# Kernel tuning notes

Hardware: AMD Instinct MI355X
Metric: run time of the kernel (lower is better)

Reference implementation:

```python
import jax, jax.numpy as jnp
import numpy as np

# CaMoE_Block MoE dispatch/combine reference.
# Assumptions (undefined submodules in source): RWKV7_TimeMix/att residual omitted
# (h = ln2(x) directly); SparseRWKVFFN experts modeled as RWKV channel-mix FFNs
# y = relu(h @ W1)^2 @ W2; the LinearTransformerExpert (last expert) uses the same
# FFN form with recon_loss = 0; per-expert confidence head conf_e = sigmoid(h @ wc_e + bc_e).
# Faithful parts: winner selection, winning-bid lookup, straight-through scale
# factor conf / (stop_grad(conf) + 1e-6), per-expert compute, scatter-combine, residual.

B, T, C = 4, 2048, 1024
E = 5            # num_rwkv_experts + 1
H = 4 * C        # FFN hidden
LN_EPS = 1e-5


def setup_inputs() -> dict:
    key = jax.random.key(0)
    ks = jax.random.split(key, 8)
    x = jax.random.normal(ks[0], (B, T, C), dtype=jnp.float32)
    winners = jax.random.randint(ks[1], (B, T), 0, E)
    gamma = jnp.ones((C,), jnp.float32)
    beta = jnp.zeros((C,), jnp.float32)
    w1 = jax.random.normal(ks[2], (E, C, H), jnp.float32) * (1.0 / np.sqrt(C))
    w2 = jax.random.normal(ks[3], (E, H, C), jnp.float32) * (1.0 / np.sqrt(H))
    wc = jax.random.normal(ks[4], (E, C), jnp.float32) * (1.0 / np.sqrt(C))
    bc = jnp.zeros((E,), jnp.float32)
    return {"x": x, "winners": winners, "gamma": gamma, "beta": beta,
            "w1": w1, "w2": w2, "wc": wc, "bc": bc}


def _layernorm(x, gamma, beta):
    mu = jnp.mean(x, axis=-1, keepdims=True)
    var = jnp.mean(jnp.square(x - mu), axis=-1, keepdims=True)
    return (x - mu) * jax.lax.rsqrt(var + LN_EPS) * gamma + beta


def reference(x, winners, gamma, beta, w1, w2, wc, bc):
    b, t, c = x.shape
    e = w1.shape[0]
    h = _layernorm(x, gamma, beta)
    hf = h.reshape(-1, c)                     # [N, C]
    win = winners.reshape(-1)                 # [N]

    # per-expert confidences (bids)
    conf = jax.nn.sigmoid(hf @ wc.T + bc)     # [N, E]
    winning_bids = jnp.take_along_axis(conf, win[:, None], axis=1)  # [N, 1]
    scale = winning_bids / (jax.lax.stop_gradient(winning_bids) + 1e-6)

    # dense all-expert FFN (squared-ReLU channel mix), then top-1 select
    k = jnp.square(jax.nn.relu(jnp.einsum('nc,ech->enh', hf, w1)))  # [E, N, H]
    y = jnp.einsum('enh,ehc->enc', k, w2)                            # [E, N, C]
    sel = jax.nn.one_hot(win, e, dtype=y.dtype)                      # [N, E]
    expert_out = jnp.einsum('ne,enc->nc', sel, y)                    # scatter-combine

    out = (expert_out * scale).reshape(b, t, c)
    return x + out
```

## Files before the change

### kernel.cpp

```cpp
#include <hip/hip_runtime.h>
#include <hip/hip_bf16.h>
#include <stdint.h>

#define N_TOK 8192
#define C_DIM 1024
#define H_DIM 4096
#define E_NUM 5
#define LN_EPS 1e-5f

typedef __hip_bfloat16 bf16;
using s8v = __attribute__((ext_vector_type(8))) short;
using f4v = __attribute__((ext_vector_type(4))) float;

__device__ __forceinline__ void async_ld16(const bf16* g, bf16* l) {
    __builtin_amdgcn_global_load_lds(
        (const __attribute__((address_space(1))) void*)g,
        (__attribute__((address_space(3))) void*)l,
        16, 0, 0);
}

__global__ void init_meta_kernel(int* meta) {
    if (threadIdx.x < 16) meta[threadIdx.x] = 0;
}

__global__ __launch_bounds__(256) void count_kernel(
    const int* __restrict__ win, int* __restrict__ meta)
{
    __shared__ int c[E_NUM];
    if (threadIdx.x < E_NUM) c[threadIdx.x] = 0;
    __syncthreads();
    int n = blockIdx.x * 256 + threadIdx.x;
    atomicAdd(&c[win[n]], 1);
    __syncthreads();
    if (threadIdx.x < E_NUM) atomicAdd(&meta[threadIdx.x], c[threadIdx.x]);
}

__global__ void scan_kernel(int* meta) {
    if (threadIdx.x == 0) {
        int off = 0;
        for (int e = 0; e < E_NUM; ++e) {
            meta[5 + e] = off;
            off += meta[e];
            meta[11 + e] = 0;
        }
        meta[5 + E_NUM] = off;
    }
}

__global__ __launch_bounds__(256) void scatter_kernel(
    const int* __restrict__ win, int* __restrict__ meta,
    int* __restrict__ idx, int* __restrict__ pos)
{
    __shared__ int c[E_NUM];
    __shared__ int base[E_NUM];
    if (threadIdx.x < E_NUM) c[threadIdx.x] = 0;
    __syncthreads();
    int n = blockIdx.x * 256 + threadIdx.x;
    int e = win[n];
    int lr = atomicAdd(&c[e], 1);
    __syncthreads();
    if (threadIdx.x < E_NUM)
        base[threadIdx.x] = atomicAdd(&meta[11 + threadIdx.x], c[threadIdx.x]);
    __syncthreads();
    int p = meta[5 + e] + base[e] + lr;
    idx[p] = n;
    pos[n] = p;
}

__global__ __launch_bounds__(256) void ln_conf_kernel(
    const float* __restrict__ x, const int* __restrict__ win,
    const float* __restrict__ gamma, const float* __restrict__ beta,
    const float* __restrict__ wc, const float* __restrict__ bc,
    const int* __restrict__ pos,
    bf16* __restrict__ hbuf, float* __restrict__ scl,
    float* __restrict__ out)
{
    int n = blockIdx.x;
    int t = threadIdx.x;
    const float* xr = x + (size_t)n * C_DIM;
    float v[4];
    float s = 0.f, ss = 0.f;
#pragma unroll
    for (int i = 0; i < 4; ++i) {
        v[i] = xr[t + i * 256];
        s += v[i];
        ss += v[i] * v[i];
    }
#pragma unroll
    for (int off = 32; off > 0; off >>= 1) {
        s  += __shfl_down(s, off);
        ss += __shfl_down(ss, off);
    }
    __shared__ float red[8];
    __shared__ float mu_s, rv_s;
    int wave = t >> 6, lane = t & 63;
    if (lane == 0) { red[wave] = s; red[4 + wave] = ss; }
    __syncthreads();
    if (t == 0) {
        float S  = red[0] + red[1] + red[2] + red[3];
        float SS = red[4] + red[5] + red[6] + red[7];
        float mu = S * (1.f / C_DIM);
        float var = SS * (1.f / C_DIM) - mu * mu;
        mu_s = mu;
        rv_s = rsqrtf(var + LN_EPS);
    }
    __syncthreads();
    float mu = mu_s, rv = rv_s;
    int e = win[n];
    int p = pos[n];
    const float* wce = wc + (size_t)e * C_DIM;
    float dot = 0.f;
#pragma unroll
    for (int i = 0; i < 4; ++i) {
        int ci = t + i * 256;
        float hv = (v[i] - mu) * rv * gamma[ci] + beta[ci];
        hbuf[(size_t)p * C_DIM + ci] = (bf16)hv;
        out[(size_t)n * C_DIM + ci] = v[i];
        dot += hv * wce[ci];
    }
#pragma unroll
    for (int off = 32; off > 0; off >>= 1) dot += __shfl_down(dot, off);
    if (lane == 0) red[wave] = dot;
    __syncthreads();
    if (t == 0) {
        float z = red[0] + red[1] + red[2] + red[3] + bc[e];
        float conf = 1.f / (1.f + expf(-z));
        scl[p] = conf / (conf + 1e-6f);
    }
}

__global__ __launch_bounds__(256) void transpose_cvt_kernel(
    const float* __restrict__ src, bf16* __restrict__ dst, int R, int S)
{
    __shared__ float tile[64][65];
    size_t ebase = (size_t)blockIdx.z * (size_t)R * (size_t)S;
    int s0 = blockIdx.x * 64;
    int r0 = blockIdx.y * 64;
    int t = threadIdx.x;
    int lr = t >> 4;
    int lc = (t & 15) * 4;
#pragma unroll
    for (int i = 0; i < 4; ++i) {
        int r = lr + i * 16;
        float4 v = *(const float4*)(src + ebase + (size_t)(r0 + r) * S + s0 + lc);
        tile[r][lc + 0] = v.x;
        tile[r][lc + 1] = v.y;
        tile[r][lc + 2] = v.z;
        tile[r][lc + 3] = v.w;
    }
    __syncthreads();
    int sc = t >> 2;
#pragma unroll
    for (int p = 0; p < 2; ++p) {
        int ch = (t & 3) + p * 4;
        bf16 vals[8];
#pragma unroll
        for (int j = 0; j < 8; ++j)
            vals[j] = (bf16)tile[ch * 8 + j][sc];
        *(s8v*)(dst + ebase + (size_t)(s0 + sc) * R + r0 + ch * 8) = *(s8v*)vals;
    }
}


__global__ __launch_bounds__(256) void gemm1_kernel(
    const bf16* __restrict__ hbuf, const bf16* __restrict__ w1t,
    const int* __restrict__ meta, bf16* __restrict__ ks)
{
    int e = blockIdx.z;
    int base_p = meta[5 + e];
    int cnt = meta[6 + e] - base_p;
    int m0 = blockIdx.y * 128;
    if (m0 >= cnt) return;
    int n0 = blockIdx.x * 128;

    __shared__ __align__(16) bf16 As[128 * 32];
    __shared__ __align__(16) bf16 Bs[128 * 32];

    int t = threadIdx.x;
    int lane = t & 63;
    int wv = t >> 6;
    int wr = wv >> 1, wcol = wv & 1;

    int i0 = (t & 7) ^ ((t >> 3) & 7);
    int srow = 2 * (t >> 3) + (i0 >> 2);
    int schk = i0 & 3;

    int r1 = min(m0 + srow, cnt - 1);
    int r2 = min(m0 + 64 + srow, cnt - 1);
    const bf16* ga1 = hbuf + (size_t)(base_p + r1) * C_DIM + schk * 8;
    const bf16* ga2 = hbuf + (size_t)(base_p + r2) * C_DIM + schk * 8;
    const bf16* wbase = w1t + (size_t)e * H_DIM * C_DIM;
    const bf16* gb1 = wbase + (size_t)(n0 + srow) * C_DIM + schk * 8;
    const bf16* gb2 = wbase + (size_t)(n0 + 64 + srow) * C_DIM + schk * 8;

    bf16* la1 = As + t * 8;
    bf16* la2 = As + 2048 + t * 8;
    bf16* lb1 = Bs + t * 8;
    bf16* lb2 = Bs + 2048 + t * 8;

    int kq = lane >> 4;
    int rhalf = (lane & 15) >> 1;
    int ifrag = ((lane & 1) << 2) | kq;
    int foff = rhalf * 64 + (ifrag ^ rhalf) * 8;
    const bf16* Af = As + wr * 2048 + foff;
    const bf16* Bf = Bs + wcol * 2048 + foff;

    f4v acc[4][4];
    f4v zero = {0.f, 0.f, 0.f, 0.f};
#pragma unroll
    for (int i = 0; i < 4; ++i)
#pragma unroll
        for (int j = 0; j < 4; ++j) acc[i][j] = zero;

    for (int kb = 0; kb < C_DIM / 32; ++kb) {
        __syncthreads();
        async_ld16(ga1, la1); ga1 += 32;
        async_ld16(ga2, la2); ga2 += 32;
        async_ld16(gb1, lb1); gb1 += 32;
        async_ld16(gb2, lb2); gb2 += 32;
        __syncthreads();
        s8v af[4], bfv[4];
#pragma unroll
        for (int mi = 0; mi < 4; ++mi)
            af[mi] = *(const s8v*)(Af + mi * 512);
#pragma unroll
        for (int ni = 0; ni < 4; ++ni)
            bfv[ni] = *(const s8v*)(Bf + ni * 512);
#pragma unroll
        for (int mi = 0; mi < 4; ++mi)
#pragma unroll
            for (int ni = 0; ni < 4; ++ni)
                acc[mi][ni] = __builtin_amdgcn_mfma_f32_16x16x32_bf16(af[mi], bfv[ni], acc[mi][ni], 0, 0, 0);
    }

#pragma unroll
    for (int mi = 0; mi < 4; ++mi) {
#pragma unroll
        for (int r = 0; r < 4; ++r) {
            int row_local = wr * 64 + mi * 16 + ((lane >> 4) << 2) + r;
            int gm = m0 + row_local;
            if (gm < cnt) {
                size_t p = (size_t)(base_p + gm);
#pragma unroll
                for (int ni = 0; ni < 4; ++ni) {
                    int col = n0 + wcol * 64 + ni * 16 + (lane & 15);
                    float v = acc[mi][ni][r];
                    float rl = fmaxf(v, 0.f);
                    ks[p * H_DIM + col] = (bf16)(rl * rl);
                }
            }
        }
    }
}

__global__ __launch_bounds__(256) void gemm2_kernel(
    const bf16* __restrict__ ks, const bf16* __restrict__ w2t,
    const int* __restrict__ idx, const int* __restrict__ meta,
    const float* __restrict__ scl, float* __restrict__ out)
{
    int z = blockIdx.z;
    int e = z >> 1;
    int kh = z & 1;
    int base_p = meta[5 + e];
    int cnt = meta[6 + e] - base_p;
    int m0 = blockIdx.y * 128;
    if (m0 >= cnt) return;
    int n0 = blockIdx.x * 128;
    int kbase = kh * (H_DIM / 2);

    __shared__ __align__(16) bf16 As[128 * 32];
    __shared__ __align__(16) bf16 Bs[128 * 32];

    int t = threadIdx.x;
    int lane = t & 63;
    int wv = t >> 6;
    int wr = wv >> 1, wcol = wv & 1;

    int i0 = (t & 7) ^ ((t >> 3) & 7);
    int srow = 2 * (t >> 3) + (i0 >> 2);
    int schk = i0 & 3;

    int r1 = min(m0 + srow, cnt - 1);
    int r2 = min(m0 + 64 + srow, cnt - 1);
    const bf16* ga1 = ks + (size_t)(base_p + r1) * H_DIM + kbase + schk * 8;
    const bf16* ga2 = ks + (size_t)(base_p + r2) * H_DIM + kbase + schk * 8;
    const bf16* wbase = w2t + (size_t)e * C_DIM * H_DIM;
    const bf16* gb1 = wbase + (size_t)(n0 + srow) * H_DIM + kbase + schk * 8;
    const bf16* gb2 = wbase + (size_t)(n0 + 64 + srow) * H_DIM + kbase + schk * 8;

    bf16* la1 = As + t * 8;
    bf16* la2 = As + 2048 + t * 8;
    bf16* lb1 = Bs + t * 8;
    bf16* lb2 = Bs + 2048 + t * 8;

    int kq = lane >> 4;
    int rhalf = (lane & 15) >> 1;
    int ifrag = ((lane & 1) << 2) | kq;
    int foff = rhalf * 64 + (ifrag ^ rhalf) * 8;
    const bf16* Af = As + wr * 2048 + foff;
    const bf16* Bf = Bs + wcol * 2048 + foff;

    f4v acc[4][4];
    f4v zero = {0.f, 0.f, 0.f, 0.f};
#pragma unroll
    for (int i = 0; i < 4; ++i)
#pragma unroll
        for (int j = 0; j < 4; ++j) acc[i][j] = zero;

    for (int kb = 0; kb < (H_DIM / 2) / 32; ++kb) {
        __syncthreads();
        async_ld16(ga1, la1); ga1 += 32;
        async_ld16(ga2, la2); ga2 += 32;
        async_ld16(gb1, lb1); gb1 += 32;
        async_ld16(gb2, lb2); gb2 += 32;
        __syncthreads();
        s8v af[4], bfv[4];
#pragma unroll
        for (int mi = 0; mi < 4; ++mi)
            af[mi] = *(const s8v*)(Af + mi * 512);
#pragma unroll
        for (int ni = 0; ni < 4; ++ni)
            bfv[ni] = *(const s8v*)(Bf + ni * 512);
#pragma unroll
        for (int mi = 0; mi < 4; ++mi)
#pragma unroll
            for (int ni = 0; ni < 4; ++ni)
                acc[mi][ni] = __builtin_amdgcn_mfma_f32_16x16x32_bf16(af[mi], bfv[ni], acc[mi][ni], 0, 0, 0);
    }

#pragma unroll
    for (int mi = 0; mi < 4; ++mi) {
        int tok[4];
        float sclv[4];
#pragma unroll
        for (int r = 0; r < 4; ++r) {
            int row_local = wr * 64 + mi * 16 + ((lane >> 4) << 2) + r;
            int gm = m0 + row_local;
            if (gm < cnt) {
                tok[r] = idx[base_p + gm];
                sclv[r] = scl[base_p + gm];
            } else {
                tok[r] = -1;
                sclv[r] = 0.f;
            }
        }
#pragma unroll
        for (int ni = 0; ni < 4; ++ni) {
            int col = n0 + wcol * 64 + ni * 16 + (lane & 15);
#pragma unroll
            for (int r = 0; r < 4; ++r) {
                if (tok[r] >= 0) {
                    size_t o = (size_t)tok[r] * C_DIM + col;
                    atomicAdd(&out[o], acc[mi][ni][r] * sclv[r]);
                }
            }
        }
    }
}

extern "C" void kernel_launch(void* const* d_in, const int* in_sizes, int n_in,
                              void* d_out, int out_size, void* d_ws, size_t ws_size,
                              hipStream_t stream) {
    const float* x     = (const float*)d_in[0];
    const int*   win   = (const int*)d_in[1];
    const float* gamma = (const float*)d_in[2];
    const float* beta  = (const float*)d_in[3];
    const float* w1    = (const float*)d_in[4];
    const float* w2    = (const float*)d_in[5];
    const float* wc    = (const float*)d_in[6];
    const float* bc    = (const float*)d_in[7];
    float* out = (float*)d_out;

    char* ws = (char*)d_ws;
    size_t o = 0;
    bf16* w1t  = (bf16*)(ws + o); o += (size_t)E_NUM * H_DIM * C_DIM * 2;
    bf16* w2t  = (bf16*)(ws + o); o += (size_t)E_NUM * C_DIM * H_DIM * 2;
    bf16* hbuf = (bf16*)(ws + o); o += (size_t)N_TOK * C_DIM * 2;
    bf16* ks   = (bf16*)(ws + o); o += (size_t)N_TOK * H_DIM * 2;
    float* scl = (float*)(ws + o); o += (size_t)N_TOK * 4;
    int* idx   = (int*)(ws + o);   o += (size_t)N_TOK * 4;
    int* pos   = (int*)(ws + o);   o += (size_t)N_TOK * 4;
    int* meta  = (int*)(ws + o);   o += 64;

    hipLaunchKernelGGL(init_meta_kernel, dim3(1), dim3(64), 0, stream, meta);
    hipLaunchKernelGGL(count_kernel, dim3(N_TOK / 256), dim3(256), 0, stream, win, meta);
    hipLaunchKernelGGL(scan_kernel, dim3(1), dim3(64), 0, stream, meta);
    hipLaunchKernelGGL(scatter_kernel, dim3(N_TOK / 256), dim3(256), 0, stream, win, meta, idx, pos);
    hipLaunchKernelGGL(transpose_cvt_kernel, dim3(H_DIM / 64, C_DIM / 64, E_NUM), dim3(256), 0, stream,
                       w1, w1t, C_DIM, H_DIM);
    hipLaunchKernelGGL(transpose_cvt_kernel, dim3(C_DIM / 64, H_DIM / 64, E_NUM), dim3(256), 0, stream,
                       w2, w2t, H_DIM, C_DIM);
    hipLaunchKernelGGL(ln_conf_kernel, dim3(N_TOK), dim3(256), 0, stream,
                       x, win, gamma, beta, wc, bc, pos, hbuf, scl, out);
    hipLaunchKernelGGL(gemm1_kernel, dim3(H_DIM / 128, 64, E_NUM), dim3(256), 0, stream,
                       hbuf, w1t, meta, ks);
    hipLaunchKernelGGL(gemm2_kernel, dim3(C_DIM / 128, 64, E_NUM * 2), dim3(256), 0, stream,
                       ks, w2t, idx, meta, scl, out);
}
```

Before: 504.6 us.

## Pipeline gemm2 with triple-buffered LDS, drop split-K atomics, remap workgroups

Result: slower. 579.4 us (+14.8%).

```diff
diff --git a/kernel.cpp b/kernel.cpp
--- a/kernel.cpp
+++ b/kernel.cpp
@@ -72,8 +72,7 @@
     const float* __restrict__ gamma, const float* __restrict__ beta,
     const float* __restrict__ wc, const float* __restrict__ bc,
     const int* __restrict__ pos,
-    bf16* __restrict__ hbuf, float* __restrict__ scl,
-    float* __restrict__ out)
+    bf16* __restrict__ hbuf, float* __restrict__ scl)
 {
     int n = blockIdx.x;
     int t = threadIdx.x;
@@ -115,7 +114,6 @@
         int ci = t + i * 256;
         float hv = (v[i] - mu) * rv * gamma[ci] + beta[ci];
         hbuf[(size_t)p * C_DIM + ci] = (bf16)hv;
-        out[(size_t)n * C_DIM + ci] = v[i];
         dot += hv * wce[ci];
     }
 #pragma unroll
@@ -166,12 +164,19 @@
     const bf16* __restrict__ hbuf, const bf16* __restrict__ w1t,
     const int* __restrict__ meta, bf16* __restrict__ ks)
 {
-    int e = blockIdx.z;
+    const int GX = H_DIM / 128;
+    const int NWG = GX * 64 * E_NUM;
+    int d = (blockIdx.z * 64 + blockIdx.y) * GX + blockIdx.x;
+    int w = (d & 7) * (NWG >> 3) + (d >> 3);
+    int bx = w & (GX - 1);
+    int by = (w / GX) & 63;
+    int e  = w / (GX * 64);
+
     int base_p = meta[5 + e];
     int cnt = meta[6 + e] - base_p;
-    int m0 = blockIdx.y * 128;
+    int m0 = by * 128;
     if (m0 >= cnt) return;
-    int n0 = blockIdx.x * 128;
+    int n0 = bx * 128;
 
     __shared__ __align__(16) bf16 As[128 * 32];
     __shared__ __align__(16) bf16 Bs[128 * 32];
@@ -256,20 +261,25 @@
 __global__ __launch_bounds__(256) void gemm2_kernel(
     const bf16* __restrict__ ks, const bf16* __restrict__ w2t,
     const int* __restrict__ idx, const int* __restrict__ meta,
-    const float* __restrict__ scl, float* __restrict__ out)
-{
-    int z = blockIdx.z;
-    int e = z >> 1;
-    int kh = z & 1;
+    const float* __restrict__ x, const float* __restrict__ scl,
+    float* __restrict__ out)
+{
+    const int GX = C_DIM / 128;
+    const int NWG = GX * 64 * E_NUM;
+    int d = (blockIdx.z * 64 + blockIdx.y) * GX + blockIdx.x;
+    int w = (d & 7) * (NWG >> 3) + (d >> 3);
+    int bx = w & (GX - 1);
+    int by = (w / GX) & 63;
+    int e  = w / (GX * 64);
+
     int base_p = meta[5 + e];
     int cnt = meta[6 + e] - base_p;
-    int m0 = blockIdx.y * 128;
+    int m0 = by * 128;
     if (m0 >= cnt) return;
-    int n0 = blockIdx.x * 128;
-    int kbase = kh * (H_DIM / 2);
-
-    __shared__ __align__(16) bf16 As[128 * 32];
-    __shared__ __align__(16) bf16 Bs[128 * 32];
+    int n0 = bx * 128;
+
+    __shared__ __align__(16) bf16 As[3][128 * 32];
+    __shared__ __align__(16) bf16 Bs[3][128 * 32];
 
     int t = threadIdx.x;
     int lane = t & 63;
@@ -282,23 +292,21 @@
 
     int r1 = min(m0 + srow, cnt - 1);
     int r2 = min(m0 + 64 + srow, cnt - 1);
-    const bf16* ga1 = ks + (size_t)(base_p + r1) * H_DIM + kbase + schk * 8;
-    const bf16* ga2 = ks + (size_t)(base_p + r2) * H_DIM + kbase + schk * 8;
+    const bf16* ga1 = ks + (size_t)(base_p + r1) * H_DIM + schk * 8;
+    const bf16* ga2 = ks + (size_t)(base_p + r2) * H_DIM + schk * 8;
     const bf16* wbase = w2t + (size_t)e * C_DIM * H_DIM;
-    const bf16* gb1 = wbase + (size_t)(n0 + srow) * H_DIM + kbase + schk * 8;
-    const bf16* gb2 = wbase + (size_t)(n0 + 64 + srow) * H_DIM + kbase + schk * 8;
-
-    bf16* la1 = As + t * 8;
-    bf16* la2 = As + 2048 + t * 8;
-    bf16* lb1 = Bs + t * 8;
-    bf16* lb2 = Bs + 2048 + t * 8;
+    const bf16* gb1 = wbase + (size_t)(n0 + srow) * H_DIM + schk * 8;
+    const bf16* gb2 = wbase + (size_t)(n0 + 64 + srow) * H_DIM + schk * 8;
+
+    int lo1 = t * 8;
+    int lo2 = 2048 + t * 8;
 
     int kq = lane >> 4;
     int rhalf = (lane & 15) >> 1;
     int ifrag = ((lane & 1) << 2) | kq;
     int foff = rhalf * 64 + (ifrag ^ rhalf) * 8;
-    const bf16* Af = As + wr * 2048 + foff;
-    const bf16* Bf = Bs + wcol * 2048 + foff;
+    int aoff = wr * 2048 + foff;
+    int boff = wcol * 2048 + foff;
 
     f4v acc[4][4];
     f4v zero = {0.f, 0.f, 0.f, 0.f};
@@ -307,25 +315,50 @@
 #pragma unroll
         for (int j = 0; j < 4; ++j) acc[i][j] = zero;
 
-    for (int kb = 0; kb < (H_DIM / 2) / 32; ++kb) {
-        __syncthreads();
-        async_ld16(ga1, la1); ga1 += 32;
-        async_ld16(ga2, la2); ga2 += 32;
-        async_ld16(gb1, lb1); gb1 += 32;
-        async_ld16(gb2, lb2); gb2 += 32;
-        __syncthreads();
+    const int nk = H_DIM / 32;
+
+#pragma unroll
+    for (int pt = 0; pt < 2; ++pt) {
+        async_ld16(ga1, &As[pt][lo1]); ga1 += 32;
+        async_ld16(ga2, &As[pt][lo2]); ga2 += 32;
+        async_ld16(gb1, &Bs[pt][lo1]); gb1 += 32;
+        async_ld16(gb2, &Bs[pt][lo2]); gb2 += 32;
+    }
+
+    int cur = 0, st = 2;
+    for (int kb = 0; kb < nk; ++kb) {
+        if (kb < nk - 2) {
+            async_ld16(ga1, &As[st][lo1]); ga1 += 32;
+            async_ld16(ga2, &As[st][lo2]); ga2 += 32;
+            async_ld16(gb1, &Bs[st][lo1]); gb1 += 32;
+            async_ld16(gb2, &Bs[st][lo2]); gb2 += 32;
+            asm volatile("s_waitcnt vmcnt(8)" ::: "memory");
+        } else if (kb == nk - 2) {
+            asm volatile("s_waitcnt vmcnt(4)" ::: "memory");
+        } else {
+            asm volatile("s_waitcnt vmcnt(0)" ::: "memory");
+        }
+        __builtin_amdgcn_s_barrier();
+
+        const bf16* Ac = &As[cur][0];
+        const bf16* Bc = &Bs[cur][0];
         s8v af[4], bfv[4];
 #pragma unroll
         for (int mi = 0; mi < 4; ++mi)
-            af[mi] = *(const s8v*)(Af + mi * 512);
+            af[mi] = *(const s8v*)(Ac + aoff + mi * 512);
 #pragma unroll
         for (int ni = 0; ni < 4; ++ni)
-            bfv[ni] = *(const s8v*)(Bf + ni * 512);
+            bfv[ni] = *(const s8v*)(Bc + boff + ni * 512);
 #pragma unroll
         for (int mi = 0; mi < 4; ++mi)
 #pragma unroll
             for (int ni = 0; ni < 4; ++ni)
                 acc[mi][ni] = __builtin_amdgcn_mfma_f32_16x16x32_bf16(af[mi], bfv[ni], acc[mi][ni], 0, 0, 0);
+
+        asm volatile("s_waitcnt lgkmcnt(0)" ::: "memory");
+        __builtin_amdgcn_s_barrier();
+        cur = (cur == 2) ? 0 : cur + 1;
+        st  = (st  == 2) ? 0 : st  + 1;
     }
 
 #pragma unroll
@@ -351,7 +384,7 @@
             for (int r = 0; r < 4; ++r) {
                 if (tok[r] >= 0) {
                     size_t o = (size_t)tok[r] * C_DIM + col;
-                    atomicAdd(&out[o], acc[mi][ni][r] * sclv[r]);
+                    out[o] = x[o] + acc[mi][ni][r] * sclv[r];
                 }
             }
         }
@@ -391,9 +424,9 @@
     hipLaunchKernelGGL(transpose_cvt_kernel, dim3(C_DIM / 64, H_DIM / 64, E_NUM), dim3(256), 0, stream,
                        w2, w2t, H_DIM, C_DIM);
     hipLaunchKernelGGL(ln_conf_kernel, dim3(N_TOK), dim3(256), 0, stream,
-                       x, win, gamma, beta, wc, bc, pos, hbuf, scl, out);
+                       x, win, gamma, beta, wc, bc, pos, hbuf, scl);
     hipLaunchKernelGGL(gemm1_kernel, dim3(H_DIM / 128, 64, E_NUM), dim3(256), 0, stream,
                        hbuf, w1t, meta, ks);
-    hipLaunchKernelGGL(gemm2_kernel, dim3(C_DIM / 128, 64, E_NUM * 2), dim3(256), 0, stream,
-                       ks, w2t, idx, meta, scl, out);
-}
+    hipLaunchKernelGGL(gemm2_kernel, dim3(C_DIM / 128, 64, E_NUM), dim3(256), 0, stream,
+                       ks, w2t, idx, meta, x, scl, out);
+}
```
